# Kernel tuning notes

Measured on AMD Instinct MI355X. Metric: run time of the kernel, lower is better.

The kernel has to match this reference:

```python
import jax, jax.numpy as jnp
import numpy as np

B, T, P, H, D = 2, 2048, 1024, 16, 128
C = H * D  # 2048
ROPE_THETA = 10000.0


def setup_inputs() -> dict:
    key = jax.random.key(0)
    ks = jax.random.split(key, 5)
    x = jax.random.normal(ks[0], (B, T, C), jnp.float32)
    w_qkv = jax.random.normal(ks[1], (C, 3 * C), jnp.float32) * 0.02  # Linear(dim, 3*dim), applied as x @ w
    w_out = jax.random.normal(ks[2], (C, C), jnp.float32) * 0.02
    past_k = jax.random.normal(ks[3], (B, H, P, D), jnp.float32)
    past_v = jax.random.normal(ks[4], (B, H, P, D), jnp.float32)
    return {"x": x, "w_qkv": w_qkv, "w_out": w_out, "past_k": past_k, "past_v": past_v}


def _rope(q, k, offset):
    # rotate-half RoPE (GPT-NeoX style), positions offset..offset+T-1
    d = q.shape[-1]
    inv_freq = 1.0 / (ROPE_THETA ** (jnp.arange(0, d, 2, dtype=jnp.float32) / d))  # [d/2]
    pos = offset + jnp.arange(q.shape[2], dtype=jnp.float32)                        # [T]
    ang = pos[:, None] * inv_freq[None, :]                                          # [T, d/2]
    cos = jnp.concatenate([jnp.cos(ang), jnp.cos(ang)], -1)[None, None]             # [1,1,T,d]
    sin = jnp.concatenate([jnp.sin(ang), jnp.sin(ang)], -1)[None, None]

    def rot_half(t):
        t1, t2 = jnp.split(t, 2, axis=-1)
        return jnp.concatenate([-t2, t1], -1)

    return q * cos + rot_half(q) * sin, k * cos + rot_half(k) * sin


def reference(x, w_qkv, w_out, past_k, past_v):
    Bv, Tv, Cv = x.shape
    Hn = past_k.shape[1]
    Dd = Cv // Hn
    # fused QKV projection
    qkv = x @ w_qkv                       # [B,T,3C]
    q, k, v = jnp.split(qkv, 3, axis=-1)  # each [B,T,C]

    def split_heads(t):
        return t.reshape(Bv, Tv, Hn, Dd).transpose(0, 2, 1, 3)  # [B,H,T,D]

    q, k, v = split_heads(q), split_heads(k), split_heads(v)
    # RoPE with offset = past length
    q, k = _rope(q, k, past_k.shape[2])
    # KV-cache concat along time axis
    k = jnp.concatenate([past_k, k], axis=2)  # [B,H,P+T,D]
    v = jnp.concatenate([past_v, v], axis=2)
    # SDPA: past_kv present -> is_causal=False, no mask (full attention)
    scale = 1.0 / jnp.sqrt(jnp.float32(Dd))
    scores = jnp.einsum('bhqd,bhkd->bhqk', q, k) * scale
    attn = jax.nn.softmax(scores, axis=-1)
    out = jnp.einsum('bhqk,bhkd->bhqd', attn, v)
    out = out.transpose(0, 2, 1, 3).reshape(Bv, Tv, Cv)
    return out @ w_out
```

## Files before the change

### kernel.cpp

```cpp
#include <hip/hip_runtime.h>
#include <stdint.h>

#define B_ 2
#define T_ 2048
#define P_ 1024
#define H_ 16
#define D_ 128
#define C_ 2048
#define S_ 3072
#define M_ 4096
#define N3_ 6144

typedef unsigned short u16;
typedef unsigned int uint32;
typedef __attribute__((ext_vector_type(8))) short short8;
typedef __attribute__((ext_vector_type(8))) __bf16 bf16x8;
typedef __attribute__((ext_vector_type(4))) float f32x4;
typedef __attribute__((ext_vector_type(16))) float f32x16;
typedef __attribute__((ext_vector_type(4))) unsigned short u16x4;
typedef __attribute__((ext_vector_type(4))) unsigned int uint4v;

#define SL2_ 0.12755883f

static __device__ __forceinline__ float bf2f(u16 h) {
    union { unsigned int u; float f; } x; x.u = ((unsigned int)h) << 16; return x.f;
}
static __device__ __forceinline__ u16 f2bf(float f) {
    return __builtin_bit_cast(u16, (__bf16)f);
}
static __device__ __forceinline__ uint32 cvtpk(float lo, float hi) {
    uint32 r;
    asm("v_cvt_pk_bf16_f32 %0, %1, %2" : "=v"(r) : "v"(lo), "v"(hi));
    return r;
}

static __device__ __forceinline__ f32x4 mfma_bf16(short8 a, short8 b, f32x4 c) {
    return __builtin_amdgcn_mfma_f32_16x16x32_bf16(
        __builtin_bit_cast(bf16x8, a), __builtin_bit_cast(bf16x8, b), c, 0, 0, 0);
}
static __device__ __forceinline__ f32x16 mfma32(short8 a, short8 b, f32x16 c) {
    return __builtin_amdgcn_mfma_f32_32x32x16_bf16(
        __builtin_bit_cast(bf16x8, a), __builtin_bit_cast(bf16x8, b), c, 0, 0, 0);
}

typedef __attribute__((address_space(3))) unsigned int lds_u32;
typedef const __attribute__((address_space(1))) unsigned int glb_u32;
static __device__ __forceinline__ void gload_lds16(const void* g, void* l) {
    __builtin_amdgcn_global_load_lds((glb_u32*)g, (lds_u32*)l, 16, 0, 0);
}

static __device__ __forceinline__ void storeC(float* p, float v) { *p = v; }
static __device__ __forceinline__ void storeC(u16* p, float v) { *p = f2bf(v); }

__global__ void __launch_bounds__(256)
prep1_kernel(const float* __restrict__ x, u16* __restrict__ Xb,
             const float* __restrict__ w_qkv, u16* __restrict__ Wqkvt,
             const float* __restrict__ w_out, u16* __restrict__ Woutt,
             float* __restrict__ cosT, float* __restrict__ sinT,
             const float* __restrict__ past_k, u16* __restrict__ Kc,
             const float* __restrict__ past_v, u16* __restrict__ Vt) {
    __shared__ __align__(16) char smem[16640];
    const int bid = blockIdx.x, tid = threadIdx.x;

    if (bid < 8192) {
        int idx = bid * 256 + tid;
        const float4 v = ((const float4*)x)[idx];
        u16x4 o;
        o.x = f2bf(v.x); o.y = f2bf(v.y); o.z = f2bf(v.z); o.w = f2bf(v.w);
        ((u16x4*)Xb)[idx] = o;
    } else if (bid < 12288) {
        const float* W; u16* Wt; int Ndim, n0, k0;
        if (bid < 11264) {
            int t = bid - 8192;
            W = w_qkv; Wt = Wqkvt; Ndim = N3_;
            n0 = (t % 96) * 64; k0 = (t / 96) * 64;
        } else {
            int t = bid - 11264;
            W = w_out; Wt = Woutt; Ndim = C_;
            n0 = (t & 31) * 64; k0 = (t >> 5) * 64;
        }
        float (*tile)[65] = (float(*)[65])smem;
#pragma unroll
        for (int i = 0; i < 16; i++) {
            int idx = tid + i * 256;
            int r = idx >> 6, c = idx & 63;
            tile[r][c] = W[(size_t)(k0 + r) * Ndim + n0 + c];
        }
        __syncthreads();
#pragma unroll
        for (int i = 0; i < 16; i++) {
            int idx = tid + i * 256;
            int r = idx >> 6, c = idx & 63;
            Wt[(size_t)(n0 + r) * C_ + k0 + c] = f2bf(tile[c][r]);
        }
    } else if (bid < 12800) {
        int idx = (bid - 12288) * 256 + tid;
        int t = idx >> 6, d = idx & 63;
        float inv = powf(10000.0f, -(float)d * (1.0f / 64.0f));
        float ang = (float)(P_ + t) * inv;
        cosT[idx] = cosf(ang);
        sinT[idx] = sinf(ang);
    } else if (bid < 16896) {
        int idx = (bid - 12800) * 256 + tid;
        int d4 = idx & 31;
        int p = (idx >> 5) & 1023;
        int bh = idx >> 15;
        const float4 v = ((const float4*)past_k)[idx];
        u16x4 o;
        o.x = f2bf(v.x); o.y = f2bf(v.y); o.z = f2bf(v.z); o.w = f2bf(v.w);
        *(u16x4*)&Kc[((size_t)bh * S_ + p) * 128 + (d4 << 2)] = o;
    } else {
        int t = bid - 16896;
        const int p0 = (t & 15) * 64, d0 = ((t >> 4) & 1) * 64, bh = t >> 5;
        float (*tile)[65] = (float(*)[65])smem;
#pragma unroll
        for (int i = 0; i < 16; i++) {
            int idx = tid + i * 256;
            int r = idx >> 6, c = idx & 63;
            tile[r][c] = past_v[((size_t)bh * P_ + p0 + r) * 128 + d0 + c];
        }
        __syncthreads();
#pragma unroll
        for (int i = 0; i < 16; i++) {
            int idx = tid + i * 256;
            int r = idx >> 6, c = idx & 63;
            Vt[((size_t)bh * 128 + d0 + r) * S_ + p0 + c] = f2bf(tile[c][r]);
        }
    }
}

__global__ void __launch_bounds__(256)
prep2_kernel(u16* __restrict__ QKVb, u16* __restrict__ Kc,
             const float* __restrict__ cosT, const float* __restrict__ sinT,
             u16* __restrict__ Vt) {
    __shared__ u16 tile[64][65];
    const int bid = blockIdx.x, tid = threadIdx.x;

    if (bid < 4096) {
        int idx = bid * 256 + tid;
        int j = idx & 15;
        int h = (idx >> 4) & 15;
        int t = (idx >> 8) & 2047;
        int b = idx >> 19;
        const int d0 = j << 2;
        size_t rowoff = (size_t)(b * T_ + t) * N3_;
        const float4 cv = *(const float4*)&cosT[(t << 6) + d0];
        const float4 sv = *(const float4*)&sinT[(t << 6) + d0];
        const float cc[4] = {cv.x, cv.y, cv.z, cv.w};
        const float ss[4] = {sv.x, sv.y, sv.z, sv.w};
        {
            u16* p = QKVb + rowoff + h * 128 + d0;
            u16x4 x1 = *(u16x4*)p, x2 = *(u16x4*)(p + 64);
            u16x4 o1, o2;
#pragma unroll
            for (int e = 0; e < 4; e++) {
                float a = bf2f(x1[e]), bb = bf2f(x2[e]);
                o1[e] = f2bf((a * cc[e] - bb * ss[e]) * SL2_);
                o2[e] = f2bf((bb * cc[e] + a * ss[e]) * SL2_);
            }
            *(u16x4*)p = o1;
            *(u16x4*)(p + 64) = o2;
        }
        {
            const u16* p = QKVb + rowoff + C_ + h * 128 + d0;
            u16x4 x1 = *(const u16x4*)p, x2 = *(const u16x4*)(p + 64);
            u16x4 o1, o2;
#pragma unroll
            for (int e = 0; e < 4; e++) {
                float a = bf2f(x1[e]), bb = bf2f(x2[e]);
                o1[e] = f2bf(a * cc[e] - bb * ss[e]);
                o2[e] = f2bf(bb * cc[e] + a * ss[e]);
            }
            u16* o = Kc + ((size_t)(b * H_ + h) * S_ + P_ + t) * 128 + d0;
            *(u16x4*)o = o1;
            *(u16x4*)(o + 64) = o2;
        }
    } else {
        int t = bid - 4096;
        const int t0 = (t & 31) * 64, d0 = ((t >> 5) & 1) * 64, bh = t >> 6;
        const int b = bh >> 4, h = bh & 15;
#pragma unroll
        for (int i = 0; i < 16; i++) {
            int idx = tid + i * 256;
            int r = idx >> 6, c = idx & 63;
            tile[r][c] = QKVb[(size_t)(b * T_ + t0 + r) * N3_ + 2 * C_ + h * 128 + d0 + c];
        }
        __syncthreads();
#pragma unroll
        for (int i = 0; i < 16; i++) {
            int idx = tid + i * 256;
            int r = idx >> 6, c = idx & 63;
            Vt[((size_t)bh * 128 + d0 + r) * S_ + P_ + t0 + c] = tile[c][r];
        }
    }
}

template <typename OutT>
__global__ void __launch_bounds__(512, 1)
gemm3(const u16* __restrict__ A, const u16* __restrict__ Bt,
      OutT* __restrict__ Co, int Mdim, int Ndim, int Kdim) {
    __shared__ u16 lA[3 * 256 * 64];
    __shared__ u16 lB[3 * 128 * 64];
    const int nbx = Ndim >> 7;
    const int nwg = (Mdim >> 8) * nbx;
    int bid = blockIdx.x;
    int wg = (bid & 7) * (nwg >> 3) + (bid >> 3);
    const int bm = wg / nbx, bn = wg % nbx;
    const int m0 = bm << 8, n0 = bn << 7;
    const int tid = threadIdx.x;
    const int wave = tid >> 6, lane = tid & 63;
    const int mw = wave >> 1, nw = wave & 1;
    const int l15 = lane & 15, l4 = lane >> 4;

    f32x4 acc[4][4];
#pragma unroll
    for (int i = 0; i < 4; i++)
#pragma unroll
        for (int j = 0; j < 4; j++) acc[i][j] = (f32x4){0.f, 0.f, 0.f, 0.f};

    const u16* aSrc[4];
    const u16* bSrc[2];
#pragma unroll
    for (int i = 0; i < 4; i++) {
        int cid = i * 512 + tid;
        int r = cid >> 3, pc = cid & 7;
        aSrc[i] = A + (size_t)(m0 + r) * Kdim + ((pc ^ (r & 7)) << 3);
    }
#pragma unroll
    for (int i = 0; i < 2; i++) {
        int cid = i * 512 + tid;
        int r = cid >> 3, pc = cid & 7;
        bSrc[i] = Bt + (size_t)(n0 + r) * Kdim + ((pc ^ (r & 7)) << 3);
    }

#define STAGE3(bi, kt) do {                                                     \
    u16* _pa = lA + (bi) * 16384 + wave * 512;                                  \
    u16* _pb = lB + (bi) * 8192 + wave * 512;                                   \
    _Pragma("unroll")                                                           \
    for (int i = 0; i < 4; i++)                                                 \
        gload_lds16(aSrc[i] + (size_t)(kt) * 64, _pa + i * 4096);               \
    _Pragma("unroll")                                                           \
    for (int i = 0; i < 2; i++)                                                 \
        gload_lds16(bSrc[i] + (size_t)(kt) * 64, _pb + i * 4096);               \
} while (0)

    STAGE3(0, 0);
    STAGE3(1, 1);

    const int NT = Kdim >> 6;
    int bc = 0;
    for (int t = 0; t < NT; ++t) {
        if (t + 1 < NT) asm volatile("s_waitcnt vmcnt(6)" ::: "memory");
        else            asm volatile("s_waitcnt vmcnt(0)" ::: "memory");
        __builtin_amdgcn_s_barrier();
        asm volatile("" ::: "memory");
        if (t + 2 < NT) {
            int b2 = bc + 2; if (b2 >= 3) b2 -= 3;
            STAGE3(b2, t + 2);
        }
        const u16* la = lA + bc * 16384;
        const u16* lb = lB + bc * 8192;
        short8 af[4][2], bf[4][2];
#pragma unroll
        for (int i = 0; i < 4; i++)
#pragma unroll
            for (int kk = 0; kk < 2; kk++) {
                int r = mw * 64 + i * 16 + l15;
                int cb = (kk * 64 + l4 * 16) ^ ((r & 7) << 4);
                af[i][kk] = *(const short8*)&la[r * 64 + (cb >> 1)];
            }
#pragma unroll
        for (int j = 0; j < 4; j++)
#pragma unroll
            for (int kk = 0; kk < 2; kk++) {
                int r = nw * 64 + j * 16 + l15;
                int cb = (kk * 64 + l4 * 16) ^ ((r & 7) << 4);
                bf[j][kk] = *(const short8*)&lb[r * 64 + (cb >> 1)];
            }
        __builtin_amdgcn_s_setprio(1);
#pragma unroll
        for (int kk = 0; kk < 2; kk++)
#pragma unroll
            for (int i = 0; i < 4; i++)
#pragma unroll
                for (int j = 0; j < 4; j++)
                    acc[i][j] = mfma_bf16(af[i][kk], bf[j][kk], acc[i][j]);
        __builtin_amdgcn_s_setprio(0);
        __builtin_amdgcn_sched_barrier(0);
        bc = bc + 1; if (bc >= 3) bc = 0;
    }
#undef STAGE3

#pragma unroll
    for (int i = 0; i < 4; i++)
#pragma unroll
        for (int j = 0; j < 4; j++) {
            int row = m0 + mw * 64 + i * 16 + (l4 << 2);
            int col = n0 + nw * 64 + j * 16 + l15;
#pragma unroll
            for (int q = 0; q < 4; q++)
                storeC(&Co[(size_t)(row + q) * Ndim + col], acc[i][j][q]);
        }
}

__global__ void __launch_bounds__(256, 2)
attn_kernel(const u16* __restrict__ QKVb, const u16* __restrict__ Kc,
            const u16* __restrict__ Vt, u16* __restrict__ O) {
    __shared__ u16 ldsK[2][64 * 128];
    __shared__ u16 ldsV[2][64 * 128];

    int bid = blockIdx.x;
    int wg = (bid & 7) * 64 + (bid >> 3);
    const int qc = wg & 15;
    const int bh = wg >> 4;
    const int b = bh >> 4, h = bh & 15;
    const int tid = threadIdx.x, wave = tid >> 6, lane = tid & 63;
    const int l31 = lane & 31, hi = lane >> 5;

    const int krow = tid >> 4;
    const int kcol = ((((tid & 15) ^ krow) << 4)) >> 1;
    const int vslog = (tid & 15) ^ (tid >> 4);
    const int vd0 = ((tid >> 4) << 1) + (vslog >> 3);
    const int vk = (vslog & 7) << 3;

    const u16* Kbh = Kc + (size_t)bh * S_ * 128;
    const u16* Vbh = Vt + (size_t)bh * 128 * S_;

    const int tq = qc * 128 + wave * 32 + l31;
    short8 qf[8];
    {
        const u16* qp = QKVb + (size_t)(b * T_ + tq) * N3_ + h * 128 + hi * 8;
#pragma unroll
        for (int ks = 0; ks < 8; ks++) qf[ks] = *(const short8*)(qp + ks * 16);
    }

    uint4v onesu = {0x3F803F80u, 0x3F803F80u, 0x3F803F80u, 0x3F803F80u};
    short8 ones8 = __builtin_bit_cast(short8, onesu);

    f32x16 acco[4];
#pragma unroll
    for (int d = 0; d < 4; d++) acco[d] = (f32x16)(0.0f);
    f32x16 accs = (f32x16)(0.0f);

#define STAGE(bufi, tt) do {                                                    \
    const int _s0 = (tt) * 64;                                                  \
    _Pragma("unroll")                                                           \
    for (int i = 0; i < 4; i++)                                                 \
        gload_lds16(Kbh + (size_t)(_s0 + krow + i * 16) * 128 + kcol,           \
                    (char*)&ldsK[bufi][0] + i * 4096 + wave * 1024);            \
    _Pragma("unroll")                                                           \
    for (int i = 0; i < 4; i++)                                                 \
        gload_lds16(Vbh + (size_t)(vd0 + i * 32) * S_ + _s0 + vk,               \
                    (char*)&ldsV[bufi][0] + i * 4096 + wave * 1024);            \
} while (0)

    STAGE(0, 0);
    __syncthreads();

    const int swzK = (l31 & 15) << 4;
    const int vprB = l31 >> 1;
    const int vhbB = (l31 & 1) << 3;

    for (int t = 0; t < S_ / 64; ++t) {
        const int cur = t & 1;
        if (t < S_ / 64 - 1) STAGE(cur ^ 1, t + 1);

        const u16* Kl = ldsK[cur];
        const u16* Vl = ldsV[cur];

        f32x16 p0 = (f32x16)(0.0f), p1 = (f32x16)(0.0f);
        __builtin_amdgcn_s_setprio(1);
#pragma unroll
        for (int ks = 0; ks < 8; ks++) {
            const int cidx = (((ks * 32 + hi * 16) ^ swzK) >> 1);
            short8 k0 = *(const short8*)&Kl[(l31 << 7) + cidx];
            short8 k1 = *(const short8*)&Kl[((32 + l31) << 7) + cidx];
            p0 = mfma32(k0, qf[ks], p0);
            p1 = mfma32(k1, qf[ks], p1);
        }
        __builtin_amdgcn_s_setprio(0);

#pragma unroll
        for (int r = 0; r < 16; r++) p0[r] = exp2f(p0[r]);
#pragma unroll
        for (int r = 0; r < 16; r++) p1[r] = exp2f(p1[r]);

        uint32 w[4][4];
#define PACK_HALF(pp, kh, ksout) do {                                           \
    uint32 A0 = cvtpk(pp[(kh)*8 + 0], pp[(kh)*8 + 1]);                          \
    uint32 A1 = cvtpk(pp[(kh)*8 + 2], pp[(kh)*8 + 3]);                          \
    uint32 B0 = cvtpk(pp[(kh)*8 + 4], pp[(kh)*8 + 5]);                          \
    uint32 B1 = cvtpk(pp[(kh)*8 + 6], pp[(kh)*8 + 7]);                          \
    uint32 sA0 = __shfl_xor(A0, 32), sA1 = __shfl_xor(A1, 32);                  \
    uint32 sB0 = __shfl_xor(B0, 32), sB1 = __shfl_xor(B1, 32);                  \
    w[ksout][0] = hi ? sB0 : A0;                                                \
    w[ksout][1] = hi ? sB1 : A1;                                                \
    w[ksout][2] = hi ? B0 : sA0;                                                \
    w[ksout][3] = hi ? B1 : sA1;                                                \
} while (0)
        PACK_HALF(p0, 0, 0);
        PACK_HALF(p0, 1, 1);
        PACK_HALF(p1, 0, 2);
        PACK_HALF(p1, 1, 3);
#undef PACK_HALF

        __builtin_amdgcn_s_setprio(1);
#pragma unroll
        for (int ks = 0; ks < 4; ks++) {
            uint4v pw = {w[ks][0], w[ks][1], w[ks][2], w[ks][3]};
            short8 pf = __builtin_bit_cast(short8, pw);
#pragma unroll
            for (int dblk = 0; dblk < 4; dblk++) {
                int pr = dblk * 16 + vprB;
                int sl = (vhbB + ks * 2 + hi) ^ vprB;
                short8 vf = *(const short8*)&Vl[(pr << 7) + (sl << 3)];
                acco[dblk] = mfma32(vf, pf, acco[dblk]);
            }
            accs = mfma32(ones8, pf, accs);
        }
        __builtin_amdgcn_s_setprio(0);

        __syncthreads();
    }
#undef STAGE

    float rl = 1.0f / accs[0];
    u16* Op = O + (size_t)(b * T_ + tq) * C_ + h * 128;
#pragma unroll
    for (int dblk = 0; dblk < 4; dblk++)
#pragma unroll
        for (int j = 0; j < 4; j++) {
            u16x4 o;
            o.x = f2bf(acco[dblk][4 * j + 0] * rl);
            o.y = f2bf(acco[dblk][4 * j + 1] * rl);
            o.z = f2bf(acco[dblk][4 * j + 2] * rl);
            o.w = f2bf(acco[dblk][4 * j + 3] * rl);
            *(u16x4*)(Op + dblk * 32 + j * 8 + hi * 4) = o;
        }
}


extern "C" void kernel_launch(void* const* d_in, const int* in_sizes, int n_in,
                              void* d_out, int out_size, void* d_ws, size_t ws_size,
                              hipStream_t stream) {
    const float* x      = (const float*)d_in[0];
    const float* w_qkv  = (const float*)d_in[1];
    const float* w_out  = (const float*)d_in[2];
    const float* past_k = (const float*)d_in[3];
    const float* past_v = (const float*)d_in[4];
    float* out = (float*)d_out;

    char* ws = (char*)d_ws;
    u16* Xb    = (u16*)(ws);
    u16* Wqkvt = (u16*)(ws + 16777216);
    u16* Woutt = (u16*)(ws + 41943040);
    u16* QKVb  = (u16*)(ws + 50331648);
    u16* Kc    = (u16*)(ws + 100663296);
    u16* Vt    = (u16*)(ws + 125829120);
    u16* O     = (u16*)(ws + 150994944);
    float* cosT = (float*)(ws + 167772160);
    float* sinT = (float*)(ws + 168296448);

    prep1_kernel<<<17920, 256, 0, stream>>>(x, Xb, w_qkv, Wqkvt, w_out, Woutt,
                                            cosT, sinT, past_k, Kc, past_v, Vt);

    gemm3<u16><<<(M_ / 256) * (N3_ / 128), 512, 0, stream>>>(Xb, Wqkvt, QKVb, M_, N3_, C_);

    prep2_kernel<<<6144, 256, 0, stream>>>(QKVb, Kc, cosT, sinT, Vt);

    attn_kernel<<<512, 256, 0, stream>>>(QKVb, Kc, Vt, O);

    gemm3<float><<<(M_ / 256) * (C_ / 128), 512, 0, stream>>>(O, Woutt, out, M_, C_, C_);
}
```

Measured before the change: 358.4 us.

## Software-pipeline attention loop: overlap next QK^T with current softmax/PV

The attention main loop is restructured so the QK^T MFMAs for tile t+1 are issued before the exp/pack/PV work of tile t. This lets the matrix units and the exp/shuffle work overlap within a wave. V gets a triple-buffered LDS slot and K stays double-buffered, with prefetch two tiles ahead. In exchange it adds LDS usage (an extra 16KB) and register pressure from holding two sets of score accumulators, which may hurt occupancy under launch_bounds(256,2).

```diff
diff --git a/kernel.cpp b/kernel.cpp
--- a/kernel.cpp
+++ b/kernel.cpp
@@ -307,7 +307,7 @@
 attn_kernel(const u16* __restrict__ QKVb, const u16* __restrict__ Kc,
             const u16* __restrict__ Vt, u16* __restrict__ O) {
     __shared__ u16 ldsK[2][64 * 128];
-    __shared__ u16 ldsV[2][64 * 128];
+    __shared__ u16 ldsV[3][64 * 128];
 
     int bid = blockIdx.x;
     int wg = (bid & 7) * 64 + (bid >> 3);
@@ -342,87 +342,108 @@
     for (int d = 0; d < 4; d++) acco[d] = (f32x16)(0.0f);
     f32x16 accs = (f32x16)(0.0f);
 
-#define STAGE(bufi, tt) do {                                                    \
-    const int _s0 = (tt) * 64;                                                  \
-    _Pragma("unroll")                                                           \
-    for (int i = 0; i < 4; i++)                                                 \
-        gload_lds16(Kbh + (size_t)(_s0 + krow + i * 16) * 128 + kcol,           \
-                    (char*)&ldsK[bufi][0] + i * 4096 + wave * 1024);            \
-    _Pragma("unroll")                                                           \
-    for (int i = 0; i < 4; i++)                                                 \
-        gload_lds16(Vbh + (size_t)(vd0 + i * 32) * S_ + _s0 + vk,               \
-                    (char*)&ldsV[bufi][0] + i * 4096 + wave * 1024);            \
-} while (0)
-
-    STAGE(0, 0);
-    __syncthreads();
-
     const int swzK = (l31 & 15) << 4;
     const int vprB = l31 >> 1;
     const int vhbB = (l31 & 1) << 3;
 
-    for (int t = 0; t < S_ / 64; ++t) {
-        const int cur = t & 1;
-        if (t < S_ / 64 - 1) STAGE(cur ^ 1, t + 1);
-
-        const u16* Kl = ldsK[cur];
-        const u16* Vl = ldsV[cur];
-
-        f32x16 p0 = (f32x16)(0.0f), p1 = (f32x16)(0.0f);
-        __builtin_amdgcn_s_setprio(1);
-#pragma unroll
-        for (int ks = 0; ks < 8; ks++) {
-            const int cidx = (((ks * 32 + hi * 16) ^ swzK) >> 1);
-            short8 k0 = *(const short8*)&Kl[(l31 << 7) + cidx];
-            short8 k1 = *(const short8*)&Kl[((32 + l31) << 7) + cidx];
-            p0 = mfma32(k0, qf[ks], p0);
-            p1 = mfma32(k1, qf[ks], p1);
-        }
-        __builtin_amdgcn_s_setprio(0);
-
-#pragma unroll
-        for (int r = 0; r < 16; r++) p0[r] = exp2f(p0[r]);
-#pragma unroll
-        for (int r = 0; r < 16; r++) p1[r] = exp2f(p1[r]);
-
-        uint32 w[4][4];
-#define PACK_HALF(pp, kh, ksout) do {                                           \
+#define STAGE(tt) do {                                                          \
+    const int _s0 = (tt) * 64;                                                  \
+    char* _kb = (char*)&ldsK[(tt) & 1][0];                                      \
+    char* _vb = (char*)&ldsV[(tt) % 3][0];                                      \
+    _Pragma("unroll")                                                           \
+    for (int i = 0; i < 4; i++)                                                 \
+        gload_lds16(Kbh + (size_t)(_s0 + krow + i * 16) * 128 + kcol,           \
+                    _kb + i * 4096 + wave * 1024);                              \
+    _Pragma("unroll")                                                           \
+    for (int i = 0; i < 4; i++)                                                 \
+        gload_lds16(Vbh + (size_t)(vd0 + i * 32) * S_ + _s0 + vk,               \
+                    _vb + i * 4096 + wave * 1024);                              \
+} while (0)
+
+#define QKT(tt, P0, P1) do {                                                    \
+    const u16* Kl = &ldsK[(tt) & 1][0];                                         \
+    (P0) = (f32x16)(0.0f); (P1) = (f32x16)(0.0f);                               \
+    __builtin_amdgcn_s_setprio(1);                                              \
+    _Pragma("unroll")                                                           \
+    for (int ks = 0; ks < 8; ks++) {                                            \
+        const int cidx = (((ks * 32 + hi * 16) ^ swzK) >> 1);                   \
+        short8 k0 = *(const short8*)&Kl[(l31 << 7) + cidx];                     \
+        short8 k1 = *(const short8*)&Kl[((32 + l31) << 7) + cidx];              \
+        (P0) = mfma32(k0, qf[ks], (P0));                                        \
+        (P1) = mfma32(k1, qf[ks], (P1));                                        \
+    }                                                                           \
+    __builtin_amdgcn_s_setprio(0);                                              \
+} while (0)
+
+#define PACK_HALF(pp, kh, ksout, W) do {                                        \
     uint32 A0 = cvtpk(pp[(kh)*8 + 0], pp[(kh)*8 + 1]);                          \
     uint32 A1 = cvtpk(pp[(kh)*8 + 2], pp[(kh)*8 + 3]);                          \
     uint32 B0 = cvtpk(pp[(kh)*8 + 4], pp[(kh)*8 + 5]);                          \
     uint32 B1 = cvtpk(pp[(kh)*8 + 6], pp[(kh)*8 + 7]);                          \
     uint32 sA0 = __shfl_xor(A0, 32), sA1 = __shfl_xor(A1, 32);                  \
     uint32 sB0 = __shfl_xor(B0, 32), sB1 = __shfl_xor(B1, 32);                  \
-    w[ksout][0] = hi ? sB0 : A0;                                                \
-    w[ksout][1] = hi ? sB1 : A1;                                                \
-    w[ksout][2] = hi ? B0 : sA0;                                                \
-    w[ksout][3] = hi ? B1 : sA1;                                                \
+    W[ksout][0] = hi ? sB0 : A0;                                                \
+    W[ksout][1] = hi ? sB1 : A1;                                                \
+    W[ksout][2] = hi ? B0 : sA0;                                                \
+    W[ksout][3] = hi ? B1 : sA1;                                                \
 } while (0)
-        PACK_HALF(p0, 0, 0);
-        PACK_HALF(p0, 1, 1);
-        PACK_HALF(p1, 0, 2);
-        PACK_HALF(p1, 1, 3);
+
+#define SMPV(tt, P0, P1) do {                                                   \
+    _Pragma("unroll")                                                           \
+    for (int r = 0; r < 16; r++) (P0)[r] = exp2f((P0)[r]);                      \
+    _Pragma("unroll")                                                           \
+    for (int r = 0; r < 16; r++) (P1)[r] = exp2f((P1)[r]);                      \
+    uint32 w[4][4];                                                             \
+    PACK_HALF((P0), 0, 0, w);                                                   \
+    PACK_HALF((P0), 1, 1, w);                                                   \
+    PACK_HALF((P1), 0, 2, w);                                                   \
+    PACK_HALF((P1), 1, 3, w);                                                   \
+    const u16* Vl = &ldsV[(tt) % 3][0];                                         \
+    __builtin_amdgcn_s_setprio(1);                                              \
+    _Pragma("unroll")                                                           \
+    for (int ks = 0; ks < 4; ks++) {                                            \
+        uint4v pw = {w[ks][0], w[ks][1], w[ks][2], w[ks][3]};                   \
+        short8 pf = __builtin_bit_cast(short8, pw);                             \
+        _Pragma("unroll")                                                       \
+        for (int dblk = 0; dblk < 4; dblk++) {                                  \
+            int pr = dblk * 16 + vprB;                                          \
+            int sl = (vhbB + ks * 2 + hi) ^ vprB;                               \
+            short8 vf = *(const short8*)&Vl[(pr << 7) + (sl << 3)];             \
+            acco[dblk] = mfma32(vf, pf, acco[dblk]);                            \
+        }                                                                       \
+        accs = mfma32(ones8, pf, accs);                                         \
+    }                                                                           \
+    __builtin_amdgcn_s_setprio(0);                                              \
+} while (0)
+
+    STAGE(0);
+    STAGE(1);
+    __syncthreads();
+
+    f32x16 pA0, pA1, pB0, pB1;
+    QKT(0, pA0, pA1);
+
+#pragma unroll 1
+    for (int i = 0; i < 23; ++i) {
+        const int t = 2 * i;
+        __syncthreads();
+        STAGE(t + 2);
+        QKT(t + 1, pB0, pB1);
+        SMPV(t, pA0, pA1);
+        __syncthreads();
+        STAGE(t + 3);
+        QKT(t + 2, pA0, pA1);
+        SMPV(t + 1, pB0, pB1);
+    }
+    __syncthreads();
+    QKT(47, pB0, pB1);
+    SMPV(46, pA0, pA1);
+    SMPV(47, pB0, pB1);
+
+#undef STAGE
+#undef QKT
 #undef PACK_HALF
-
-        __builtin_amdgcn_s_setprio(1);
-#pragma unroll
-        for (int ks = 0; ks < 4; ks++) {
-            uint4v pw = {w[ks][0], w[ks][1], w[ks][2], w[ks][3]};
-            short8 pf = __builtin_bit_cast(short8, pw);
-#pragma unroll
-            for (int dblk = 0; dblk < 4; dblk++) {
-                int pr = dblk * 16 + vprB;
-                int sl = (vhbB + ks * 2 + hi) ^ vprB;
-                short8 vf = *(const short8*)&Vl[(pr << 7) + (sl << 3)];
-                acco[dblk] = mfma32(vf, pf, acco[dblk]);
-            }
-            accs = mfma32(ones8, pf, accs);
-        }
-        __builtin_amdgcn_s_setprio(0);
-
-        __syncthreads();
-    }
-#undef STAGE
+#undef SMPV
 
     float rl = 1.0f / accs[0];
     u16* Op = O + (size_t)(b * T_ + tq) * C_ + h * 128;
```

Measured after the change: 357.0 us, median of 3. No clear change (-0.4%).

## Pre-swizzle V into MFMA fragment layout and load it directly from global

Applied to the files above, without the earlier changes.

The prep kernels now write V in a fragment-major layout, so each lane's 8-element MFMA operand sits contiguously and the attention kernel can load V straight from global/L2 into registers. This drops the V LDS staging buffer, halving LDS use and allowing 3 workgroups per CU. The row-sum accumulation also moves from an extra MFMA against a ones vector to scalar adds plus a cross-half shuffle. The trade is that V reads are no longer shared through LDS across waves, which raises global and L2 traffic and adds load latency to the PV loop.

```diff
diff --git a/kernel.cpp b/kernel.cpp
--- a/kernel.cpp
+++ b/kernel.cpp
@@ -52,13 +52,14 @@
 static __device__ __forceinline__ void storeC(float* p, float v) { *p = v; }
 static __device__ __forceinline__ void storeC(u16* p, float v) { *p = f2bf(v); }
 
+
 __global__ void __launch_bounds__(256)
 prep1_kernel(const float* __restrict__ x, u16* __restrict__ Xb,
              const float* __restrict__ w_qkv, u16* __restrict__ Wqkvt,
              const float* __restrict__ w_out, u16* __restrict__ Woutt,
              float* __restrict__ cosT, float* __restrict__ sinT,
              const float* __restrict__ past_k, u16* __restrict__ Kc,
-             const float* __restrict__ past_v, u16* __restrict__ Vt) {
+             const float* __restrict__ past_v, u16* __restrict__ V4) {
     __shared__ __align__(16) char smem[16640];
     const int bid = blockIdx.x, tid = threadIdx.x;
 
@@ -120,11 +121,23 @@
             tile[r][c] = past_v[((size_t)bh * P_ + p0 + r) * 128 + d0 + c];
         }
         __syncthreads();
-#pragma unroll
-        for (int i = 0; i < 16; i++) {
+        const int t_tile = p0 >> 6;
+#pragma unroll
+        for (int i = 0; i < 2; i++) {
             int idx = tid + i * 256;
-            int r = idx >> 6, c = idx & 63;
-            Vt[((size_t)bh * 128 + d0 + r) * S_ + p0 + c] = f2bf(tile[c][r]);
+            int dl = idx >> 3, c8 = idx & 7;
+            int d = d0 + dl;
+            int ks = c8 >> 1, h2 = c8 & 1;
+            size_t frag = ((size_t)(bh * 48 + t_tile) * 16 + ks * 4 + (d >> 5));
+            u16* dst = V4 + frag * 512 + ((h2 << 5) + (d & 31)) * 8;
+            u16x4 lo, hh;
+#pragma unroll
+            for (int e = 0; e < 4; e++) {
+                lo[e] = f2bf(tile[c8 * 8 + e][dl]);
+                hh[e] = f2bf(tile[c8 * 8 + 4 + e][dl]);
+            }
+            *(u16x4*)dst = lo;
+            *(u16x4*)(dst + 4) = hh;
         }
     }
 }
@@ -132,7 +145,7 @@
 __global__ void __launch_bounds__(256)
 prep2_kernel(u16* __restrict__ QKVb, u16* __restrict__ Kc,
              const float* __restrict__ cosT, const float* __restrict__ sinT,
-             u16* __restrict__ Vt) {
+             u16* __restrict__ V4) {
     __shared__ u16 tile[64][65];
     const int bid = blockIdx.x, tid = threadIdx.x;
 
@@ -186,11 +199,23 @@
             tile[r][c] = QKVb[(size_t)(b * T_ + t0 + r) * N3_ + 2 * C_ + h * 128 + d0 + c];
         }
         __syncthreads();
-#pragma unroll
-        for (int i = 0; i < 16; i++) {
+        const int t_tile = (P_ + t0) >> 6;
+#pragma unroll
+        for (int i = 0; i < 2; i++) {
             int idx = tid + i * 256;
-            int r = idx >> 6, c = idx & 63;
-            Vt[((size_t)bh * 128 + d0 + r) * S_ + P_ + t0 + c] = tile[c][r];
+            int dl = idx >> 3, c8 = idx & 7;
+            int d = d0 + dl;
+            int ks = c8 >> 1, h2 = c8 & 1;
+            size_t frag = ((size_t)(bh * 48 + t_tile) * 16 + ks * 4 + (d >> 5));
+            u16* dst = V4 + frag * 512 + ((h2 << 5) + (d & 31)) * 8;
+            u16x4 lo, hh;
+#pragma unroll
+            for (int e = 0; e < 4; e++) {
+                lo[e] = tile[c8 * 8 + e][dl];
+                hh[e] = tile[c8 * 8 + 4 + e][dl];
+            }
+            *(u16x4*)dst = lo;
+            *(u16x4*)(dst + 4) = hh;
         }
     }
 }
@@ -303,11 +328,10 @@
         }
 }
 
-__global__ void __launch_bounds__(256, 2)
+__global__ void __launch_bounds__(256, 3)
 attn_kernel(const u16* __restrict__ QKVb, const u16* __restrict__ Kc,
-            const u16* __restrict__ Vt, u16* __restrict__ O) {
+            const u16* __restrict__ V4, u16* __restrict__ O) {
     __shared__ u16 ldsK[2][64 * 128];
-    __shared__ u16 ldsV[2][64 * 128];
 
     int bid = blockIdx.x;
     int wg = (bid & 7) * 64 + (bid >> 3);
@@ -319,12 +343,9 @@
 
     const int krow = tid >> 4;
     const int kcol = ((((tid & 15) ^ krow) << 4)) >> 1;
-    const int vslog = (tid & 15) ^ (tid >> 4);
-    const int vd0 = ((tid >> 4) << 1) + (vslog >> 3);
-    const int vk = (vslog & 7) << 3;
 
     const u16* Kbh = Kc + (size_t)bh * S_ * 128;
-    const u16* Vbh = Vt + (size_t)bh * 128 * S_;
+    const u16* V4l = V4 + (size_t)bh * 48 * 8192 + lane * 8;
 
     const int tq = qc * 128 + wave * 32 + l31;
     short8 qf[8];
@@ -334,39 +355,36 @@
         for (int ks = 0; ks < 8; ks++) qf[ks] = *(const short8*)(qp + ks * 16);
     }
 
-    uint4v onesu = {0x3F803F80u, 0x3F803F80u, 0x3F803F80u, 0x3F803F80u};
-    short8 ones8 = __builtin_bit_cast(short8, onesu);
-
     f32x16 acco[4];
 #pragma unroll
     for (int d = 0; d < 4; d++) acco[d] = (f32x16)(0.0f);
-    f32x16 accs = (f32x16)(0.0f);
-
-#define STAGE(bufi, tt) do {                                                    \
+    float lrow = 0.f;
+
+#define STAGEK(bufi, tt) do {                                                   \
     const int _s0 = (tt) * 64;                                                  \
     _Pragma("unroll")                                                           \
     for (int i = 0; i < 4; i++)                                                 \
         gload_lds16(Kbh + (size_t)(_s0 + krow + i * 16) * 128 + kcol,           \
                     (char*)&ldsK[bufi][0] + i * 4096 + wave * 1024);            \
-    _Pragma("unroll")                                                           \
-    for (int i = 0; i < 4; i++)                                                 \
-        gload_lds16(Vbh + (size_t)(vd0 + i * 32) * S_ + _s0 + vk,               \
-                    (char*)&ldsV[bufi][0] + i * 4096 + wave * 1024);            \
 } while (0)
 
-    STAGE(0, 0);
+    STAGEK(0, 0);
     __syncthreads();
 
     const int swzK = (l31 & 15) << 4;
-    const int vprB = l31 >> 1;
-    const int vhbB = (l31 & 1) << 3;
 
     for (int t = 0; t < S_ / 64; ++t) {
         const int cur = t & 1;
-        if (t < S_ / 64 - 1) STAGE(cur ^ 1, t + 1);
-
-        const u16* Kl = ldsK[cur];
-        const u16* Vl = ldsV[cur];
+        const u16* ft = V4l + t * 8192;
+
+        short8 va[4], vb[4];
+#pragma unroll
+        for (int dblk = 0; dblk < 4; dblk++)
+            va[dblk] = *(const short8*)(ft + dblk * 512);
+
+        if (t < S_ / 64 - 1) STAGEK(cur ^ 1, t + 1);
+
+        const u16* Kl = &ldsK[cur][0];
 
         f32x16 p0 = (f32x16)(0.0f), p1 = (f32x16)(0.0f);
         __builtin_amdgcn_s_setprio(1);
@@ -380,10 +398,24 @@
         }
         __builtin_amdgcn_s_setprio(0);
 
-#pragma unroll
-        for (int r = 0; r < 16; r++) p0[r] = exp2f(p0[r]);
-#pragma unroll
-        for (int r = 0; r < 16; r++) p1[r] = exp2f(p1[r]);
+        float s0a = 0.f, s1a = 0.f, s2a = 0.f, s3a = 0.f;
+#pragma unroll
+        for (int r = 0; r < 16; r += 4) {
+            p0[r + 0] = exp2f(p0[r + 0]); s0a += p0[r + 0];
+            p0[r + 1] = exp2f(p0[r + 1]); s1a += p0[r + 1];
+            p0[r + 2] = exp2f(p0[r + 2]); s2a += p0[r + 2];
+            p0[r + 3] = exp2f(p0[r + 3]); s3a += p0[r + 3];
+        }
+#pragma unroll
+        for (int r = 0; r < 16; r += 4) {
+            p1[r + 0] = exp2f(p1[r + 0]); s0a += p1[r + 0];
+            p1[r + 1] = exp2f(p1[r + 1]); s1a += p1[r + 1];
+            p1[r + 2] = exp2f(p1[r + 2]); s2a += p1[r + 2];
+            p1[r + 3] = exp2f(p1[r + 3]); s3a += p1[r + 3];
+        }
+        float sum = (s0a + s1a) + (s2a + s3a);
+        sum += __shfl_xor(sum, 32);
+        lrow += sum;
 
         uint32 w[4][4];
 #define PACK_HALF(pp, kh, ksout) do {                                           \
@@ -405,26 +437,44 @@
 #undef PACK_HALF
 
         __builtin_amdgcn_s_setprio(1);
-#pragma unroll
-        for (int ks = 0; ks < 4; ks++) {
-            uint4v pw = {w[ks][0], w[ks][1], w[ks][2], w[ks][3]};
-            short8 pf = __builtin_bit_cast(short8, pw);
-#pragma unroll
-            for (int dblk = 0; dblk < 4; dblk++) {
-                int pr = dblk * 16 + vprB;
-                int sl = (vhbB + ks * 2 + hi) ^ vprB;
-                short8 vf = *(const short8*)&Vl[(pr << 7) + (sl << 3)];
-                acco[dblk] = mfma32(vf, pf, acco[dblk]);
-            }
-            accs = mfma32(ones8, pf, accs);
+        {
+#pragma unroll
+            for (int dblk = 0; dblk < 4; dblk++)
+                vb[dblk] = *(const short8*)(ft + (4 + dblk) * 512);
+            uint4v pw0 = {w[0][0], w[0][1], w[0][2], w[0][3]};
+            short8 pf0 = __builtin_bit_cast(short8, pw0);
+#pragma unroll
+            for (int dblk = 0; dblk < 4; dblk++)
+                acco[dblk] = mfma32(va[dblk], pf0, acco[dblk]);
+#pragma unroll
+            for (int dblk = 0; dblk < 4; dblk++)
+                va[dblk] = *(const short8*)(ft + (8 + dblk) * 512);
+            uint4v pw1 = {w[1][0], w[1][1], w[1][2], w[1][3]};
+            short8 pf1 = __builtin_bit_cast(short8, pw1);
+#pragma unroll
+            for (int dblk = 0; dblk < 4; dblk++)
+                acco[dblk] = mfma32(vb[dblk], pf1, acco[dblk]);
+#pragma unroll
+            for (int dblk = 0; dblk < 4; dblk++)
+                vb[dblk] = *(const short8*)(ft + (12 + dblk) * 512);
+            uint4v pw2 = {w[2][0], w[2][1], w[2][2], w[2][3]};
+            short8 pf2 = __builtin_bit_cast(short8, pw2);
+#pragma unroll
+            for (int dblk = 0; dblk < 4; dblk++)
+                acco[dblk] = mfma32(va[dblk], pf2, acco[dblk]);
+            uint4v pw3 = {w[3][0], w[3][1], w[3][2], w[3][3]};
+            short8 pf3 = __builtin_bit_cast(short8, pw3);
+#pragma unroll
+            for (int dblk = 0; dblk < 4; dblk++)
+                acco[dblk] = mfma32(vb[dblk], pf3, acco[dblk]);
         }
         __builtin_amdgcn_s_setprio(0);
 
         __syncthreads();
     }
-#undef STAGE
-
-    float rl = 1.0f / accs[0];
+#undef STAGEK
+
+    float rl = 1.0f / lrow;
     u16* Op = O + (size_t)(b * T_ + tq) * C_ + h * 128;
 #pragma unroll
     for (int dblk = 0; dblk < 4; dblk++)
@@ -456,19 +506,19 @@
     u16* Woutt = (u16*)(ws + 41943040);
     u16* QKVb  = (u16*)(ws + 50331648);
     u16* Kc    = (u16*)(ws + 100663296);
-    u16* Vt    = (u16*)(ws + 125829120);
+    u16* V4    = (u16*)(ws + 125829120);
     u16* O     = (u16*)(ws + 150994944);
     float* cosT = (float*)(ws + 167772160);
     float* sinT = (float*)(ws + 168296448);
 
     prep1_kernel<<<17920, 256, 0, stream>>>(x, Xb, w_qkv, Wqkvt, w_out, Woutt,
-                                            cosT, sinT, past_k, Kc, past_v, Vt);
+                                            cosT, sinT, past_k, Kc, past_v, V4);
 
     gemm3<u16><<<(M_ / 256) * (N3_ / 128), 512, 0, stream>>>(Xb, Wqkvt, QKVb, M_, N3_, C_);
 
-    prep2_kernel<<<6144, 256, 0, stream>>>(QKVb, Kc, cosT, sinT, Vt);
-
-    attn_kernel<<<512, 256, 0, stream>>>(QKVb, Kc, Vt, O);
+    prep2_kernel<<<6144, 256, 0, stream>>>(QKVb, Kc, cosT, sinT, V4);
+
+    attn_kernel<<<512, 256, 0, stream>>>(QKVb, Kc, V4, O);
 
     gemm3<float><<<(M_ / 256) * (C_ / 128), 512, 0, stream>>>(O, Woutt, out, M_, C_, C_);
 }
```

Result: slower. 533.3 us (+48.8%).
